# Kernel optimization log

Hardware: AMD Instinct MI355X
Metric: run time of the kernel (lower is better)

## Reference

```python
import jax, jax.numpy as jnp
import numpy as np
import math

NUM_HEADS = 16

def setup_inputs() -> dict:
    key = jax.random.key(0)
    ks = jax.random.split(key, 5)
    d_model = 1024
    std = math.sqrt(2.0 / (d_model + d_model))
    x = jax.random.normal(ks[0], (2, 2048, d_model), dtype=jnp.float32)
    Wq = jax.random.normal(ks[1], (d_model, d_model), dtype=jnp.float32) * std
    Wk = jax.random.normal(ks[2], (d_model, d_model), dtype=jnp.float32) * std
    Wv = jax.random.normal(ks[3], (d_model, d_model), dtype=jnp.float32) * std
    Wo = jax.random.normal(ks[4], (d_model, d_model), dtype=jnp.float32) * std
    return {"x": x, "Wq": Wq, "Wk": Wk, "Wv": Wv, "Wo": Wo}

def reference(x, Wq, Wk, Wv, Wo):
    # x: [b, s, d]; W*: [d_out, d_in]
    b, s, d = x.shape
    h = NUM_HEADS
    dh = d // h
    def proj(W):
        y = jnp.einsum('bsd,ed->bse', x, W)           # [b, s, d]
        return y.reshape(b, s, h, dh).transpose(0, 2, 1, 3)  # [b, h, s, dh]
    Q, K, V = proj(Wq), proj(Wk), proj(Wv)
    scale = 1.0 / math.sqrt(dh)
    logits = jnp.einsum('bhqd,bhkd->bhqk', Q, K) * scale  # [b, h, s, s]
    causal = jnp.tril(jnp.ones((s, s), dtype=bool))
    logits = jnp.where(causal, logits, -jnp.inf)
    attn = jax.nn.softmax(logits, axis=-1)
    out = jnp.einsum('bhqk,bhkd->bhqd', attn, V)          # [b, h, s, dh]
    out = out.transpose(0, 2, 1, 3).reshape(b, s, d)
    return jnp.einsum('bsv,dv->bsd', out, Wo)
```

## Files before the change

kernel.cpp:

```cpp
#include <hip/hip_runtime.h>
#include <hip/hip_bf16.h>
#include <math.h>

typedef unsigned short ushort_t;
typedef __attribute__((ext_vector_type(8))) short bf16x8;
typedef __attribute__((ext_vector_type(4))) float f32x4;

#define MFMA16(a,b,c) __builtin_amdgcn_mfma_f32_16x16x32_bf16(a,b,c,0,0,0)
#define QSCALE 0.1803368801111204f

typedef unsigned int u32;
typedef __attribute__((address_space(1))) const u32* gp1_t;
typedef __attribute__((address_space(3))) u32* lp3_t;

__device__ __forceinline__ void async_copy16(void* l, const void* g) {
    __builtin_amdgcn_global_load_lds((gp1_t)g, (lp3_t)l, 16, 0, 0);
}

__device__ __forceinline__ ushort_t f2bf(float f) {
    unsigned u = __float_as_uint(f);
    unsigned r = u + 0x7fffu + ((u >> 16) & 1u);
    return (ushort_t)(r >> 16);
}

__global__ __launch_bounds__(256) void cvt_kernel(
    const float* __restrict__ x,  const float* __restrict__ wq,
    const float* __restrict__ wk, const float* __restrict__ wv,
    const float* __restrict__ wo, ushort_t* __restrict__ dst)
{
    size_t base = ((size_t)blockIdx.x * 256 + threadIdx.x) * 8;
    const float* src; size_t off;
    if      (base < 4194304ul) { src = x;  off = base; }
    else if (base < 5242880ul) { src = wq; off = base - 4194304ul; }
    else if (base < 6291456ul) { src = wk; off = base - 5242880ul; }
    else if (base < 7340032ul) { src = wv; off = base - 6291456ul; }
    else                       { src = wo; off = base - 7340032ul; }
    float4 a = *(const float4*)(src + off);
    float4 b = *(const float4*)(src + off + 4);
    struct alignas(16) U8 { ushort_t v[8]; } o;
    o.v[0]=f2bf(a.x); o.v[1]=f2bf(a.y); o.v[2]=f2bf(a.z); o.v[3]=f2bf(a.w);
    o.v[4]=f2bf(b.x); o.v[5]=f2bf(b.y); o.v[6]=f2bf(b.z); o.v[7]=f2bf(b.w);
    *(U8*)(dst + base) = o;
}

__global__ __launch_bounds__(512) void gemm_bt(
    const ushort_t* __restrict__ A, const ushort_t* __restrict__ B,
    ushort_t* __restrict__ Oq, ushort_t* __restrict__ Ok,
    ushort_t* __restrict__ Ovt, float* __restrict__ Of, int is_out)
{
    __shared__ ushort_t As[2][128 * 64];
    __shared__ ushort_t Bs[2][128 * 64];
    const int t = threadIdx.x, l = t & 63, w = t >> 6;
    const int l4 = l >> 4, lm = l & 15;
    const int wr = w >> 1, wc = w & 1;

    const int nwg = gridDim.x * gridDim.y;
    const int orig = (int)blockIdx.y * gridDim.x + (int)blockIdx.x;
    const int qq = nwg >> 3;
    const int swz = (orig & 7) * qq + (orig >> 3);
    const int n0 = (swz % gridDim.x) * 128;
    const int m0 = (swz / gridDim.x) * 128;

    const int srow = t >> 3, scol = t & 7;

    f32x4 acc[2][4] = {};

    #pragma unroll
    for (int i = 0; i < 2; ++i) {
        const int row = i * 64 + srow;
        const int c = scol ^ (row & 7);
        async_copy16((char*)&As[0][0] + i * 8192 + t * 16,
                     A + (size_t)(m0 + row) * 1024 + c * 8);
        async_copy16((char*)&Bs[0][0] + i * 8192 + t * 16,
                     B + (size_t)(n0 + row) * 1024 + c * 8);
    }

    for (int kt = 0; kt < 16; ++kt) {
        const int cur = kt & 1;
        if (kt + 1 < 16) {
            const int k0 = (kt + 1) * 64;
            #pragma unroll
            for (int i = 0; i < 2; ++i) {
                const int row = i * 64 + srow;
                const int c = scol ^ (row & 7);
                async_copy16((char*)&As[cur ^ 1][0] + i * 8192 + t * 16,
                             A + (size_t)(m0 + row) * 1024 + k0 + c * 8);
                async_copy16((char*)&Bs[cur ^ 1][0] + i * 8192 + t * 16,
                             B + (size_t)(n0 + row) * 1024 + k0 + c * 8);
            }
            asm volatile("s_waitcnt vmcnt(4)" ::: "memory");
        } else {
            asm volatile("s_waitcnt vmcnt(0)" ::: "memory");
        }
        __builtin_amdgcn_s_barrier();

        #pragma unroll
        for (int ks = 0; ks < 2; ++ks) {
            bf16x8 af[2], bfr[4];
            #pragma unroll
            for (int mi = 0; mi < 2; ++mi) {
                const int row = wr * 32 + mi * 16 + lm;
                const int ch = l4 + 4 * ks;
                af[mi] = *(const bf16x8*)(&As[cur][0] + row * 64 + ((ch ^ (row & 7)) << 3));
            }
            #pragma unroll
            for (int ni = 0; ni < 4; ++ni) {
                const int row = wc * 64 + ni * 16 + lm;
                const int ch = l4 + 4 * ks;
                bfr[ni] = *(const bf16x8*)(&Bs[cur][0] + row * 64 + ((ch ^ (row & 7)) << 3));
            }
            #pragma unroll
            for (int mi = 0; mi < 2; ++mi)
                #pragma unroll
                for (int ni = 0; ni < 4; ++ni)
                    acc[mi][ni] = MFMA16(af[mi], bfr[ni], acc[mi][ni]);
        }
        asm volatile("s_waitcnt lgkmcnt(0)" ::: "memory");
        __builtin_amdgcn_s_barrier();
    }

    const int mb = m0 + wr * 32, nb = n0 + wc * 64;
    if (is_out) {
        #pragma unroll
        for (int mi = 0; mi < 2; ++mi)
            #pragma unroll
            for (int ni = 0; ni < 4; ++ni) {
                const int n = nb + ni * 16 + lm;
                const int mr = mb + mi * 16 + l4 * 4;
                #pragma unroll
                for (int r = 0; r < 4; ++r)
                    Of[(size_t)(mr + r) * 1024 + n] = acc[mi][ni][r];
            }
    } else if (nb >= 2048) {
        #pragma unroll
        for (int mi = 0; mi < 2; ++mi)
            #pragma unroll
            for (int ni = 0; ni < 4; ++ni) {
                const int nv = nb - 2048 + ni * 16 + lm;
                const int m = mb + mi * 16 + l4 * 4;
                const int b = m >> 11, s = m & 2047, h = nv >> 6, d = nv & 63;
                ushort4 pk;
                pk.x = f2bf(acc[mi][ni][0]); pk.y = f2bf(acc[mi][ni][1]);
                pk.z = f2bf(acc[mi][ni][2]); pk.w = f2bf(acc[mi][ni][3]);
                *(ushort4*)(Ovt + (((size_t)(b * 16 + h) * 64 + d) * 2048 + s)) = pk;
            }
    } else {
        ushort_t* O = (nb < 1024) ? Oq : Ok;
        const float qs = (nb < 1024) ? (float)QSCALE : 1.0f;
        const int nbase = nb & 1023;
        #pragma unroll
        for (int mi = 0; mi < 2; ++mi)
            #pragma unroll
            for (int ni = 0; ni < 4; ++ni) {
                const int n = nbase + ni * 16 + lm;
                const int h = n >> 6, d = n & 63;
                #pragma unroll
                for (int r = 0; r < 4; ++r) {
                    const int m = mb + mi * 16 + l4 * 4 + r;
                    const int b = m >> 11, s = m & 2047;
                    O[((size_t)(b * 16 + h) * 2048 + s) * 64 + d] =
                        f2bf(acc[mi][ni][r] * qs);
                }
            }
    }
}

template<bool MASK>
__device__ __forceinline__ void attn_tile2(
    const ushort_t* Kbuf, const ushort_t* Vbuf, ushort_t* Pw,
    const bf16x8 (&qf)[2][2], const bf16x8 ones,
    f32x4 (&o)[2][4], f32x4 (&ol)[2], float (&m_run)[2],
    int kv0, int q0w, int l4, int lm)
{
    f32x4 sf[2][4] = {};
    #pragma unroll
    for (int ks = 0; ks < 2; ++ks)
        #pragma unroll
        for (int cf = 0; cf < 4; ++cf) {
            const int rowK = cf * 16 + lm;
            const int ch = l4 + 4 * ks;
            bf16x8 kf = *(const bf16x8*)(Kbuf + rowK * 64 + ((ch ^ (rowK & 7)) << 3));
            sf[0][cf] = MFMA16(kf, qf[0][ks], sf[0][cf]);
            sf[1][cf] = MFMA16(kf, qf[1][ks], sf[1][cf]);
        }

    float tmax[2] = {-1e30f, -1e30f};
    #pragma unroll
    for (int qi = 0; qi < 2; ++qi) {
        const int qrow = q0w + qi * 16 + lm;
        #pragma unroll
        for (int cf = 0; cf < 4; ++cf)
            #pragma unroll
            for (int r = 0; r < 4; ++r) {
                float v = sf[qi][cf][r];
                if (MASK && (kv0 + cf * 16 + l4 * 4 + r > qrow)) v = -30000.f;
                sf[qi][cf][r] = v;
                tmax[qi] = fmaxf(tmax[qi], v);
            }
        tmax[qi] = fmaxf(tmax[qi], __shfl_xor(tmax[qi], 16));
        tmax[qi] = fmaxf(tmax[qi], __shfl_xor(tmax[qi], 32));
    }

    if (!__all(fmaxf(tmax[0] - m_run[0], tmax[1] - m_run[1]) <= 8.f)) {
        #pragma unroll
        for (int qi = 0; qi < 2; ++qi) {
            const float mn = fmaxf(m_run[qi], tmax[qi]);
            const float alpha = __builtin_amdgcn_exp2f(m_run[qi] - mn);
            #pragma unroll
            for (int df = 0; df < 4; ++df)
                #pragma unroll
                for (int r = 0; r < 4; ++r)
                    o[qi][df][r] *= alpha;
            #pragma unroll
            for (int r = 0; r < 4; ++r) ol[qi][r] *= alpha;
            m_run[qi] = mn;
        }
    }

    #pragma unroll
    for (int qi = 0; qi < 2; ++qi)
        #pragma unroll
        for (int cf = 0; cf < 4; ++cf) {
            float p0 = __builtin_amdgcn_exp2f(sf[qi][cf][0] - m_run[qi]);
            float p1 = __builtin_amdgcn_exp2f(sf[qi][cf][1] - m_run[qi]);
            float p2 = __builtin_amdgcn_exp2f(sf[qi][cf][2] - m_run[qi]);
            float p3 = __builtin_amdgcn_exp2f(sf[qi][cf][3] - m_run[qi]);
            __hip_bfloat162 b01 = __float22bfloat162_rn(make_float2(p0, p1));
            __hip_bfloat162 b23 = __float22bfloat162_rn(make_float2(p2, p3));
            uint2 pkv;
            __builtin_memcpy(&pkv.x, &b01, 4);
            __builtin_memcpy(&pkv.y, &b23, 4);
            *(uint2*)&Pw[(qi * 16 + lm) * 72 + cf * 16 + l4 * 4] = pkv;
        }

    #pragma unroll
    for (int ks = 0; ks < 2; ++ks) {
        bf16x8 pf0 = *(const bf16x8*)&Pw[(0 * 16 + lm) * 72 + ks * 32 + l4 * 8];
        bf16x8 pf1 = *(const bf16x8*)&Pw[(1 * 16 + lm) * 72 + ks * 32 + l4 * 8];
        #pragma unroll
        for (int df = 0; df < 4; ++df) {
            const int rowV = df * 16 + lm;
            const int ch = l4 + 4 * ks;
            bf16x8 vf = *(const bf16x8*)(Vbuf + rowV * 64 + ((ch ^ (rowV & 7)) << 3));
            o[0][df] = MFMA16(vf, pf0, o[0][df]);
            o[1][df] = MFMA16(vf, pf1, o[1][df]);
        }
        ol[0] = MFMA16(ones, pf0, ol[0]);
        ol[1] = MFMA16(ones, pf1, ol[1]);
    }
}

__global__ __launch_bounds__(512) void attn_kernel(
    const ushort_t* __restrict__ Qg, const ushort_t* __restrict__ Kg,
    const ushort_t* __restrict__ Vtg, ushort_t* __restrict__ Og)
{
    __shared__ ushort_t smem[51200];
    ushort_t* Ksm = smem;
    ushort_t* Vsm = smem + 16384;
    ushort_t* Psm = smem + 32768;

    const int t = threadIdx.x, l = t & 63, w = t >> 6;
    const int l4 = l >> 4, lm = l & 15;
    const int kvg = w >> 2, qg = w & 3;
    const int bh = blockIdx.x;
    const int qt = 15 - (int)blockIdx.y;
    const int q0 = qt * 128, q0w = q0 + qg * 32;

    const ushort_t* Kbh = Kg + (size_t)bh * 2048 * 64;
    const ushort_t* Vbh = Vtg + (size_t)bh * 64 * 2048;

    bf16x8 qf[2][2];
    #pragma unroll
    for (int qi = 0; qi < 2; ++qi) {
        const ushort_t* qp = Qg + ((size_t)bh * 2048 + q0w + qi * 16 + lm) * 64 + l4 * 8;
        qf[qi][0] = *(const bf16x8*)qp;
        qf[qi][1] = *(const bf16x8*)(qp + 32);
    }
    bf16x8 ones;
    #pragma unroll
    for (int i = 0; i < 8; ++i) ones[i] = (short)0x3F80;

    f32x4 o[2][4] = {};
    f32x4 ol[2] = {};
    float m_run[2] = {-1e30f, -1e30f};

    const int tg = t & 255;
    const int sr0 = tg >> 3, sc0 = tg & 7;
    const ushort_t* kp[2]; const ushort_t* vp[2];
    char* kd[2]; char* vd[2];
    #pragma unroll
    for (int i = 0; i < 2; ++i) {
        const int row = i * 32 + sr0;
        const int c = sc0 ^ (row & 7);
        kp[i] = Kbh + row * 64 + c * 8;
        vp[i] = Vbh + (size_t)row * 2048 + c * 8;
        kd[i] = (char*)Ksm + kvg * 16384 + i * 4096 + tg * 16;
        vd[i] = (char*)Vsm + kvg * 16384 + i * 4096 + tg * 16;
    }
    ushort_t* Pw = Psm + w * 2304;
    const ushort_t* Kgrp = Ksm + kvg * 8192;
    const ushort_t* Vgrp = Vsm + kvg * 8192;

    const int nst = qt + 1;
    {
        const int kv0p = kvg * 64;
        #pragma unroll
        for (int i = 0; i < 2; ++i) {
            async_copy16(kd[i], kp[i] + (size_t)kv0p * 64);
            async_copy16(vd[i], vp[i] + kv0p);
        }
    }

    for (int s = 0; s < nst; ++s) {
        const int cur = s & 1;
        if (s + 1 < nst) {
            const int kv0n = (2 * (s + 1) + kvg) * 64;
            #pragma unroll
            for (int i = 0; i < 2; ++i) {
                async_copy16(kd[i] + (cur ^ 1) * 8192, kp[i] + (size_t)kv0n * 64);
                async_copy16(vd[i] + (cur ^ 1) * 8192, vp[i] + kv0n);
            }
            asm volatile("s_waitcnt vmcnt(4)" ::: "memory");
        } else {
            asm volatile("s_waitcnt vmcnt(0)" ::: "memory");
        }
        __builtin_amdgcn_s_barrier();

        const int kv0 = (2 * s + kvg) * 64;
        if ((s + 1 < nst) || (q0w + 31 >= kv0)) {
            if (s + 1 < nst)
                attn_tile2<false>(Kgrp + cur * 4096, Vgrp + cur * 4096, Pw,
                                  qf, ones, o, ol, m_run, kv0, q0w, l4, lm);
            else
                attn_tile2<true>(Kgrp + cur * 4096, Vgrp + cur * 4096, Pw,
                                 qf, ones, o, ol, m_run, kv0, q0w, l4, lm);
        }
        asm volatile("s_waitcnt lgkmcnt(0)" ::: "memory");
        __builtin_amdgcn_s_barrier();
    }

    float* sc = (float*)smem;
    const int mb_ = (qg * 64 + l) * 37;
    if (kvg == 1) {
        #pragma unroll
        for (int qi = 0; qi < 2; ++qi) {
            #pragma unroll
            for (int df = 0; df < 4; ++df)
                #pragma unroll
                for (int r = 0; r < 4; ++r)
                    sc[mb_ + qi * 18 + df * 4 + r] = o[qi][df][r];
            sc[mb_ + qi * 18 + 16] = ol[qi][0];
            sc[mb_ + qi * 18 + 17] = m_run[qi];
        }
    }
    __syncthreads();
    if (kvg == 0) {
        const int b = bh >> 4, h = bh & 15;
        #pragma unroll
        for (int qi = 0; qi < 2; ++qi) {
            const float mB = sc[mb_ + qi * 18 + 17];
            const float lB = sc[mb_ + qi * 18 + 16];
            const float m = fmaxf(m_run[qi], mB);
            const float aA = __builtin_amdgcn_exp2f(m_run[qi] - m);
            const float aB = __builtin_amdgcn_exp2f(mB - m);
            const float inv = 1.f / (ol[qi][0] * aA + lB * aB);
            const int srow_o = q0w + qi * 16 + lm;
            #pragma unroll
            for (int df = 0; df < 4; ++df) {
                ushort4 pk4;
                float v0 = (o[qi][df][0] * aA + sc[mb_ + qi * 18 + df * 4 + 0] * aB) * inv;
                float v1 = (o[qi][df][1] * aA + sc[mb_ + qi * 18 + df * 4 + 1] * aB) * inv;
                float v2 = (o[qi][df][2] * aA + sc[mb_ + qi * 18 + df * 4 + 2] * aB) * inv;
                float v3 = (o[qi][df][3] * aA + sc[mb_ + qi * 18 + df * 4 + 3] * aB) * inv;
                pk4.x = f2bf(v0); pk4.y = f2bf(v1); pk4.z = f2bf(v2); pk4.w = f2bf(v3);
                *(ushort4*)&Og[((size_t)(b * 2048 + srow_o)) * 1024 + h * 64 + df * 16 + l4 * 4] = pk4;
            }
        }
    }
}

extern "C" void kernel_launch(void* const* d_in, const int* in_sizes, int n_in,
                              void* d_out, int out_size, void* d_ws, size_t ws_size,
                              hipStream_t stream)
{
    const float* x  = (const float*)d_in[0];
    const float* Wq = (const float*)d_in[1];
    const float* Wk = (const float*)d_in[2];
    const float* Wv = (const float*)d_in[3];
    const float* Wo = (const float*)d_in[4];

    ushort_t* ws  = (ushort_t*)d_ws;
    ushort_t* xb  = ws;
    ushort_t* wqb = ws + 4194304;
    ushort_t* wob = ws + 7340032;
    ushort_t* Qw  = ws + 8388608;
    ushort_t* Kw  = ws + 12582912;
    ushort_t* Vtw = ws + 16777216;
    ushort_t* Aow = ws + 20971520;

    cvt_kernel<<<4096, 256, 0, stream>>>(x, Wq, Wk, Wv, Wo, ws);
    gemm_bt<<<dim3(24, 32), 512, 0, stream>>>(xb, wqb, Qw, Kw, Vtw, nullptr, 0);
    attn_kernel<<<dim3(32, 16), 512, 0, stream>>>(Qw, Kw, Vtw, Aow);
    gemm_bt<<<dim3(8, 32), 512, 0, stream>>>(Aow, wob, nullptr, nullptr, nullptr,
                                             (float*)d_out, 1);
}
```

Measured before the change: 105.9 us.

## Use 256x256 tiled GEMM kernel for fused QKV projection

Adds a dedicated QKV projection kernel with 256x256 output tiles per 512-thread block. It interleaves async global-to-LDS prefetch of the next K slice with MFMA on the current one, in four sub-phases with barriers and s_setprio. The larger tile halves operand reloads per output but drops the grid to 192 blocks, fewer than the CU count, and uses 128 KB of LDS per block. The output-projection GEMM is simplified to a float-only epilogue.

```diff
diff --git a/kernel.cpp b/kernel.cpp
--- a/kernel.cpp
+++ b/kernel.cpp
@@ -43,10 +43,134 @@
     *(U8*)(dst + base) = o;
 }
 
+__global__ __launch_bounds__(512) void gemm256(
+    const ushort_t* __restrict__ A, const ushort_t* __restrict__ B,
+    ushort_t* __restrict__ Oq, ushort_t* __restrict__ Ok,
+    ushort_t* __restrict__ Ovt)
+{
+    __shared__ ushort_t As[2][256 * 64];
+    __shared__ ushort_t Bs[2][256 * 64];
+    const int t = threadIdx.x, l = t & 63, w = t >> 6;
+    const int l4 = l >> 4, lm = l & 15;
+    const int wr = w >> 2, wc = w & 3;
+
+    const int nwg = gridDim.x * gridDim.y;
+    const int orig = (int)blockIdx.y * gridDim.x + (int)blockIdx.x;
+    const int qq = nwg >> 3;
+    const int swz = (orig & 7) * qq + (orig >> 3);
+    const int n0 = (swz % gridDim.x) * 256;
+    const int m0 = (swz / gridDim.x) * 256;
+
+    const int srow = t >> 3, scol = t & 7;
+
+    f32x4 acc[8][4] = {};
+
+    #pragma unroll
+    for (int i = 0; i < 4; ++i) {
+        const int row = i * 64 + srow;
+        const int c = scol ^ (row & 7);
+        async_copy16((char*)&As[0][0] + i * 8192 + t * 16,
+                     A + (size_t)(m0 + row) * 1024 + c * 8);
+        async_copy16((char*)&Bs[0][0] + i * 8192 + t * 16,
+                     B + (size_t)(n0 + row) * 1024 + c * 8);
+    }
+    asm volatile("s_waitcnt vmcnt(0)" ::: "memory");
+    __builtin_amdgcn_s_barrier();
+
+    for (int kt = 0; kt < 16; ++kt) {
+        const int cur = kt & 1;
+        const int k0n = (kt + 1) * 64;
+        bf16x8 bfr[4][2];
+        #pragma unroll
+        for (int p = 0; p < 4; ++p) {
+            if (kt + 1 < 16) {
+                const int row = p * 64 + srow;
+                const int c = scol ^ (row & 7);
+                async_copy16((char*)&As[cur ^ 1][0] + p * 8192 + t * 16,
+                             A + (size_t)(m0 + row) * 1024 + k0n + c * 8);
+                async_copy16((char*)&Bs[cur ^ 1][0] + p * 8192 + t * 16,
+                             B + (size_t)(n0 + row) * 1024 + k0n + c * 8);
+            }
+            if (p == 0) {
+                if (kt + 1 < 16)
+                    asm volatile("s_waitcnt vmcnt(2)" ::: "memory");
+                else
+                    asm volatile("s_waitcnt vmcnt(0)" ::: "memory");
+                __builtin_amdgcn_s_barrier();
+                #pragma unroll
+                for (int ni = 0; ni < 4; ++ni)
+                    #pragma unroll
+                    for (int ks = 0; ks < 2; ++ks) {
+                        const int row = wc * 64 + ni * 16 + lm;
+                        const int ch = l4 + 4 * ks;
+                        bfr[ni][ks] = *(const bf16x8*)(&Bs[cur][0] + row * 64 +
+                                      ((ch ^ (row & 7)) << 3));
+                    }
+            }
+            bf16x8 af[2][2];
+            #pragma unroll
+            for (int mi2 = 0; mi2 < 2; ++mi2)
+                #pragma unroll
+                for (int ks = 0; ks < 2; ++ks) {
+                    const int row = wr * 128 + (p * 2 + mi2) * 16 + lm;
+                    const int ch = l4 + 4 * ks;
+                    af[mi2][ks] = *(const bf16x8*)(&As[cur][0] + row * 64 +
+                                  ((ch ^ (row & 7)) << 3));
+                }
+            if (p != 0) __builtin_amdgcn_s_barrier();
+            __builtin_amdgcn_s_setprio(1);
+            #pragma unroll
+            for (int ks = 0; ks < 2; ++ks)
+                #pragma unroll
+                for (int mi2 = 0; mi2 < 2; ++mi2)
+                    #pragma unroll
+                    for (int ni = 0; ni < 4; ++ni)
+                        acc[p * 2 + mi2][ni] =
+                            MFMA16(af[mi2][ks], bfr[ni][ks], acc[p * 2 + mi2][ni]);
+            __builtin_amdgcn_s_setprio(0);
+            __builtin_amdgcn_s_barrier();
+        }
+    }
+
+    const int mbw = m0 + wr * 128;
+    const int nb = n0 + wc * 64;
+    if (nb >= 2048) {
+        #pragma unroll
+        for (int mi = 0; mi < 8; ++mi)
+            #pragma unroll
+            for (int ni = 0; ni < 4; ++ni) {
+                const int nv = nb - 2048 + ni * 16 + lm;
+                const int m = mbw + mi * 16 + l4 * 4;
+                const int b = m >> 11, s = m & 2047, h = nv >> 6, d = nv & 63;
+                ushort4 pk;
+                pk.x = f2bf(acc[mi][ni][0]); pk.y = f2bf(acc[mi][ni][1]);
+                pk.z = f2bf(acc[mi][ni][2]); pk.w = f2bf(acc[mi][ni][3]);
+                *(ushort4*)(Ovt + (((size_t)(b * 16 + h) * 64 + d) * 2048 + s)) = pk;
+            }
+    } else {
+        ushort_t* O = (nb < 1024) ? Oq : Ok;
+        const float qs = (nb < 1024) ? (float)QSCALE : 1.0f;
+        const int nbase = nb & 1023;
+        #pragma unroll
+        for (int mi = 0; mi < 8; ++mi)
+            #pragma unroll
+            for (int ni = 0; ni < 4; ++ni) {
+                const int n = nbase + ni * 16 + lm;
+                const int h = n >> 6, d = n & 63;
+                #pragma unroll
+                for (int r = 0; r < 4; ++r) {
+                    const int m = mbw + mi * 16 + l4 * 4 + r;
+                    const int b = m >> 11, s = m & 2047;
+                    O[((size_t)(b * 16 + h) * 2048 + s) * 64 + d] =
+                        f2bf(acc[mi][ni][r] * qs);
+                }
+            }
+    }
+}
+
 __global__ __launch_bounds__(512) void gemm_bt(
     const ushort_t* __restrict__ A, const ushort_t* __restrict__ B,
-    ushort_t* __restrict__ Oq, ushort_t* __restrict__ Ok,
-    ushort_t* __restrict__ Ovt, float* __restrict__ Of, int is_out)
+    float* __restrict__ Of)
 {
     __shared__ ushort_t As[2][128 * 64];
     __shared__ ushort_t Bs[2][128 * 64];
@@ -120,49 +244,16 @@
     }
 
     const int mb = m0 + wr * 32, nb = n0 + wc * 64;
-    if (is_out) {
-        #pragma unroll
-        for (int mi = 0; mi < 2; ++mi)
-            #pragma unroll
-            for (int ni = 0; ni < 4; ++ni) {
-                const int n = nb + ni * 16 + lm;
-                const int mr = mb + mi * 16 + l4 * 4;
-                #pragma unroll
-                for (int r = 0; r < 4; ++r)
-                    Of[(size_t)(mr + r) * 1024 + n] = acc[mi][ni][r];
-            }
-    } else if (nb >= 2048) {
-        #pragma unroll
-        for (int mi = 0; mi < 2; ++mi)
-            #pragma unroll
-            for (int ni = 0; ni < 4; ++ni) {
-                const int nv = nb - 2048 + ni * 16 + lm;
-                const int m = mb + mi * 16 + l4 * 4;
-                const int b = m >> 11, s = m & 2047, h = nv >> 6, d = nv & 63;
-                ushort4 pk;
-                pk.x = f2bf(acc[mi][ni][0]); pk.y = f2bf(acc[mi][ni][1]);
-                pk.z = f2bf(acc[mi][ni][2]); pk.w = f2bf(acc[mi][ni][3]);
-                *(ushort4*)(Ovt + (((size_t)(b * 16 + h) * 64 + d) * 2048 + s)) = pk;
-            }
-    } else {
-        ushort_t* O = (nb < 1024) ? Oq : Ok;
-        const float qs = (nb < 1024) ? (float)QSCALE : 1.0f;
-        const int nbase = nb & 1023;
-        #pragma unroll
-        for (int mi = 0; mi < 2; ++mi)
-            #pragma unroll
-            for (int ni = 0; ni < 4; ++ni) {
-                const int n = nbase + ni * 16 + lm;
-                const int h = n >> 6, d = n & 63;
-                #pragma unroll
-                for (int r = 0; r < 4; ++r) {
-                    const int m = mb + mi * 16 + l4 * 4 + r;
-                    const int b = m >> 11, s = m & 2047;
-                    O[((size_t)(b * 16 + h) * 2048 + s) * 64 + d] =
-                        f2bf(acc[mi][ni][r] * qs);
-                }
-            }
-    }
+    #pragma unroll
+    for (int mi = 0; mi < 2; ++mi)
+        #pragma unroll
+        for (int ni = 0; ni < 4; ++ni) {
+            const int n = nb + ni * 16 + lm;
+            const int mr = mb + mi * 16 + l4 * 4;
+            #pragma unroll
+            for (int r = 0; r < 4; ++r)
+                Of[(size_t)(mr + r) * 1024 + n] = acc[mi][ni][r];
+        }
 }
 
 template<bool MASK>
@@ -399,8 +490,7 @@
     ushort_t* Aow = ws + 20971520;
 
     cvt_kernel<<<4096, 256, 0, stream>>>(x, Wq, Wk, Wv, Wo, ws);
-    gemm_bt<<<dim3(24, 32), 512, 0, stream>>>(xb, wqb, Qw, Kw, Vtw, nullptr, 0);
+    gemm256<<<dim3(12, 16), 512, 0, stream>>>(xb, wqb, Qw, Kw, Vtw);
     attn_kernel<<<dim3(32, 16), 512, 0, stream>>>(Qw, Kw, Vtw, Aow);
-    gemm_bt<<<dim3(8, 32), 512, 0, stream>>>(Aow, wob, nullptr, nullptr, nullptr,
-                                             (float*)d_out, 1);
-}
+    gemm_bt<<<dim3(8, 32), 512, 0, stream>>>(Aow, wob, (float*)d_out);
+}
```

Result: slower. 121.4 us (+14.7%).
